# Kernel optimization log

Measured on AMD Instinct MI355X. Metric: run time of the kernel, lower is better.

Reference implementation:

```python
import jax, jax.numpy as jnp
import numpy as np

B, N, D, H = 256, 64, 128, 64

def _w(key, shape, fan_in):
    return jax.random.normal(key, shape, jnp.float32) * (1.0 / np.sqrt(fan_in))

def setup_inputs() -> dict:
    key = jax.random.key(0)
    ks = jax.random.split(key, 6)
    return {
        "observations": jax.random.normal(ks[0], (B, N, D), jnp.float32),
        "enc_w": _w(ks[1], (D, H), D), "enc_b": jnp.zeros((H,), jnp.float32),
        "gate_w1": _w(ks[2], (2 * H, H), 2 * H), "gate_b1": jnp.zeros((H,), jnp.float32),
        "gate_w2": _w(ks[3], (H, 1), H), "gate_b2": jnp.zeros((1,), jnp.float32),
        "msg_w1": _w(ks[4], (H, H), H), "msg_b1": jnp.zeros((H,), jnp.float32),
        "msg_w2": _w(ks[5], (H, H), H), "msg_b2": jnp.zeros((H,), jnp.float32),
    }

def reference(observations, enc_w, enc_b, gate_w1, gate_b1, gate_w2, gate_b2,
              msg_w1, msg_b1, msg_w2, msg_b2):
    # encoder: (B, N, H)
    enc = jax.nn.relu(observations @ enc_w + enc_b)
    h = enc.shape[-1]
    # gate layer 1 on concat([e_i, e_j]) == e_i @ W_top + e_j @ W_bot; avoids
    # materializing the (B, N, N, 2H) concat tensor.
    w_i, w_j = gate_w1[:h], gate_w1[h:]
    gi = enc @ w_i                       # (B, N, H) contribution of receiver i
    gj = enc @ w_j + gate_b1             # (B, N, H) contribution of sender j
    hid = jax.nn.relu(gi[:, :, None, :] + gj[:, None, :, :])   # (B, N, N, H)
    gates = jax.nn.sigmoid(jnp.squeeze(hid @ gate_w2, -1) + gate_b2[0])  # (B, N, N)
    # message_gen(encoded): identical for every i in the original loop
    msg = jax.nn.relu(enc @ msg_w1 + msg_b1) @ msg_w2 + msg_b2  # (B, N, H)
    # enhanced[b, i] = sum_j gates[b, i, j] * msg[b, j]
    enhanced = jnp.einsum('bij,bjh->bih', gates, msg)           # (B, N, H)
    return enhanced
```

## Files before the change

kernel.cpp:

```cpp
#include <hip/hip_runtime.h>

typedef float  f32x4  __attribute__((ext_vector_type(4)));
typedef short  bf16x8 __attribute__((ext_vector_type(8)));

#define Bb 256
#define Nn 64
#define Dd 128
#define Hh 64

__device__ __forceinline__ uint cvtpk(float lo, float hi) {
    uint r;
    asm("v_cvt_pk_bf16_f32 %0, %1, %2" : "=v"(r) : "v"(lo), "v"(hi));
    return r;
}

union U8 { uint u[4]; bf16x8 v; };

__global__ __launch_bounds__(1024) void gcm_kernel(
    const float* __restrict__ obs,
    const float* __restrict__ enc_w,
    const float* __restrict__ enc_b,
    const float* __restrict__ gate_w1,
    const float* __restrict__ gate_b1,
    const float* __restrict__ gate_w2,
    const float* __restrict__ gate_b2,
    const float* __restrict__ msg_w1,
    const float* __restrict__ msg_b1,
    const float* __restrict__ msg_w2,
    const float* __restrict__ msg_b2,
    float* __restrict__ out)
{
    const int bb   = blockIdx.x;
    const int t    = threadIdx.x;
    const int lane = t & 63;
    const int wv   = t >> 6;
    const int lr   = lane & 15;
    const int lg   = lane >> 4;
    const int rt   = wv & 3;
    const int ct   = wv >> 2;

    __shared__ __align__(16) ushort s_encwT[Hh * Dd];
    __shared__ __align__(16) ushort s_wT[256 * Hh];
    __shared__ __align__(16) ushort s_enc  [Nn * Hh];
    __shared__ __align__(16) ushort s_msgh [Nn * Hh];
    __shared__ __align__(16) ushort s_gatesb[Nn * Hh];
    __shared__ __align__(16) ushort s_msgT [Hh * Nn];
    __shared__ __align__(16) float  s_gi[Nn * Hh];
    __shared__ __align__(16) float  s_gj[Nn * Hh];
    __shared__ __align__(16) float  s_w2[Hh];

    float4 pf[8];
    {
        const float* ob = obs + ((size_t)bb * Nn + rt * 16 + lr) * Dd + lg * 8;
        #pragma unroll
        for (int ks = 0; ks < 4; ++ks) {
            pf[2 * ks]     = *(const float4*)(ob + ks * 32);
            pf[2 * ks + 1] = *(const float4*)(ob + ks * 32 + 4);
        }
    }

    if (t < Hh) s_w2[t] = gate_w2[t];

    #pragma unroll
    for (int it = 0; it < 2; ++it) {
        const int g  = t + it * 1024;
        const int k  = g >> 4;
        const int n0 = (g & 15) * 4;
        float4 w4 = *(const float4*)(enc_w + k * Hh + n0);
        uint pA = cvtpk(w4.x, w4.y), pB = cvtpk(w4.z, w4.w);
        s_encwT[((n0 + 0) * Dd + k) ^ (((n0 + 0) & 7) << 3)] = (ushort)pA;
        s_encwT[((n0 + 1) * Dd + k) ^ (((n0 + 1) & 7) << 3)] = (ushort)(pA >> 16);
        s_encwT[((n0 + 2) * Dd + k) ^ (((n0 + 2) & 7) << 3)] = (ushort)pB;
        s_encwT[((n0 + 3) * Dd + k) ^ (((n0 + 3) & 7) << 3)] = (ushort)(pB >> 16);
    }

    bf16x8 afrag[4];
    #pragma unroll
    for (int ks = 0; ks < 4; ++ks) {
        U8 u;
        u.u[0] = cvtpk(pf[2 * ks].x,     pf[2 * ks].y);
        u.u[1] = cvtpk(pf[2 * ks].z,     pf[2 * ks].w);
        u.u[2] = cvtpk(pf[2 * ks + 1].x, pf[2 * ks + 1].y);
        u.u[3] = cvtpk(pf[2 * ks + 1].z, pf[2 * ks + 1].w);
        afrag[ks] = u.v;
    }

    float4 pfw[4];
    {
        const int k  = t >> 4;
        const int n0 = (t & 15) * 4;
        const float* s0 = gate_w1 + k * Hh + n0;
        const float* s1 = gate_w1 + (Hh + k) * Hh + n0;
        const float* s2 = msg_w1 + k * Hh + n0;
        const float* s3 = msg_w2 + k * Hh + n0;
        pfw[0] = *(const float4*)s0;
        pfw[1] = *(const float4*)s1;
        pfw[2] = *(const float4*)s2;
        pfw[3] = *(const float4*)s3;
    }

    __syncthreads();

    {
        f32x4 acc = (f32x4){0.f, 0.f, 0.f, 0.f};
        const int n = ct * 16 + lr;
        #pragma unroll
        for (int ks = 0; ks < 4; ++ks) {
            const int k0 = ks * 32 + lg * 8;
            bf16x8 bf = *(const bf16x8*)(s_encwT + ((n * Dd + k0) ^ ((n & 7) << 3)));
            acc = __builtin_amdgcn_mfma_f32_16x16x32_bf16(afrag[ks], bf, acc, 0, 0, 0);
        }
        #pragma unroll
        for (int it = 0; it < 4; ++it) {
            const int k  = t >> 4;
            const int n0 = it * 64 + (t & 15) * 4;
            uint pA = cvtpk(pfw[it].x, pfw[it].y), pB = cvtpk(pfw[it].z, pfw[it].w);
            s_wT[((n0 + 0) * Hh + k) ^ (((n0 + 0) & 7) << 3)] = (ushort)pA;
            s_wT[((n0 + 1) * Hh + k) ^ (((n0 + 1) & 7) << 3)] = (ushort)(pA >> 16);
            s_wT[((n0 + 2) * Hh + k) ^ (((n0 + 2) & 7) << 3)] = (ushort)pB;
            s_wT[((n0 + 3) * Hh + k) ^ (((n0 + 3) & 7) << 3)] = (ushort)(pB >> 16);
        }
        const float be = enc_b[n];
        float v0 = fmaxf(acc[0] + be, 0.f), v1 = fmaxf(acc[1] + be, 0.f);
        float v2 = fmaxf(acc[2] + be, 0.f), v3 = fmaxf(acc[3] + be, 0.f);
        uint pA = cvtpk(v0, v1), pB = cvtpk(v2, v3);
        const int rb = rt * 16 + lg * 4;
        s_enc[((rb + 0) * Hh + n) ^ (((rb + 0) & 7) << 3)] = (ushort)pA;
        s_enc[((rb + 1) * Hh + n) ^ (((rb + 1) & 7) << 3)] = (ushort)(pA >> 16);
        s_enc[((rb + 2) * Hh + n) ^ (((rb + 2) & 7) << 3)] = (ushort)pB;
        s_enc[((rb + 3) * Hh + n) ^ (((rb + 3) & 7) << 3)] = (ushort)(pB >> 16);
    }
    __syncthreads();

    {
        f32x4 acc[3];
        #pragma unroll
        for (int q = 0; q < 3; ++q) acc[q] = (f32x4){0.f, 0.f, 0.f, 0.f};
        const int arow = rt * 16 + lr;
        #pragma unroll
        for (int ks = 0; ks < 2; ++ks) {
            const int k0 = ks * 32 + lg * 8;
            bf16x8 a = *(const bf16x8*)(s_enc + ((arow * Hh + k0) ^ ((arow & 7) << 3)));
            #pragma unroll
            for (int q = 0; q < 3; ++q) {
                const int n = (ct * 3 + q) * 16 + lr;
                bf16x8 bf = *(const bf16x8*)(s_wT + ((n * Hh + k0) ^ ((n & 7) << 3)));
                acc[q] = __builtin_amdgcn_mfma_f32_16x16x32_bf16(a, bf, acc[q], 0, 0, 0);
            }
        }
        const int rb = rt * 16 + lg * 4;
        #pragma unroll
        for (int q = 0; q < 3; ++q) {
            const int nfull = (ct * 3 + q) * 16;
            const int cc = nfull + lr;
            if (nfull < 64) {
                #pragma unroll
                for (int rr = 0; rr < 4; ++rr) {
                    const int row = rb + rr;
                    s_gi[(row * Hh + cc) ^ ((row & 7) << 2)] = acc[q][rr];
                }
            } else if (nfull < 128) {
                const float b1 = gate_b1[cc - 64];
                #pragma unroll
                for (int rr = 0; rr < 4; ++rr) {
                    const int row = rb + rr;
                    s_gj[(row * Hh + (cc - 64)) ^ ((row & 7) << 2)] = acc[q][rr] + b1;
                }
            } else {
                const float bm = msg_b1[cc - 128];
                float v0 = fmaxf(acc[q][0] + bm, 0.f), v1 = fmaxf(acc[q][1] + bm, 0.f);
                float v2 = fmaxf(acc[q][2] + bm, 0.f), v3 = fmaxf(acc[q][3] + bm, 0.f);
                uint pA = cvtpk(v0, v1), pB = cvtpk(v2, v3);
                const int c2 = cc - 128;
                s_msgh[((rb + 0) * Hh + c2) ^ (((rb + 0) & 7) << 3)] = (ushort)pA;
                s_msgh[((rb + 1) * Hh + c2) ^ (((rb + 1) & 7) << 3)] = (ushort)(pA >> 16);
                s_msgh[((rb + 2) * Hh + c2) ^ (((rb + 2) & 7) << 3)] = (ushort)pB;
                s_msgh[((rb + 3) * Hh + c2) ^ (((rb + 3) & 7) << 3)] = (ushort)(pB >> 16);
            }
        }
    }
    __syncthreads();

    {
        f32x4 acc = (f32x4){0.f, 0.f, 0.f, 0.f};
        const int arow = rt * 16 + lr;
        const int n = 192 + ct * 16 + lr;
        #pragma unroll
        for (int ks = 0; ks < 2; ++ks) {
            const int k0 = ks * 32 + lg * 8;
            bf16x8 a = *(const bf16x8*)(s_msgh + ((arow * Hh + k0) ^ ((arow & 7) << 3)));
            bf16x8 bf = *(const bf16x8*)(s_wT + ((n * Hh + k0) ^ ((n & 7) << 3)));
            acc = __builtin_amdgcn_mfma_f32_16x16x32_bf16(a, bf, acc, 0, 0, 0);
        }
        const int h  = ct * 16 + lr;
        const int jb = rt * 16 + lg * 4;
        const float bm2 = msg_b2[h];
        uint pA = cvtpk(acc[0] + bm2, acc[1] + bm2);
        uint pB = cvtpk(acc[2] + bm2, acc[3] + bm2);
        const int e = (h * Nn + jb) ^ ((h & 7) << 3);
        *(uint*)(s_msgT + e)     = pA;
        *(uint*)(s_msgT + e + 2) = pB;
    }

    {
        const int row0g = wv * 4;
        float ag[4] = {0.f, 0.f, 0.f, 0.f};
        #pragma unroll 4
        for (int h0 = 0; h0 < Hh; h0 += 4) {
            float4 gj4 = *(const float4*)&s_gj[(lane * Hh + h0) ^ ((lane & 7) << 2)];
            float4 w24 = *(const float4*)&s_w2[h0];
            #pragma unroll
            for (int r = 0; r < 4; ++r) {
                const int row = row0g + r;
                float4 gi4 = *(const float4*)&s_gi[(row * Hh + h0) ^ ((row & 7) << 2)];
                ag[r] = fmaf(fmaxf(gi4.x + gj4.x, 0.f), w24.x, ag[r]);
                ag[r] = fmaf(fmaxf(gi4.y + gj4.y, 0.f), w24.y, ag[r]);
                ag[r] = fmaf(fmaxf(gi4.z + gj4.z, 0.f), w24.z, ag[r]);
                ag[r] = fmaf(fmaxf(gi4.w + gj4.w, 0.f), w24.w, ag[r]);
            }
        }
        const float b2v = gate_b2[0];
        float g0 = 1.f / (1.f + __expf(-(ag[0] + b2v)));
        float g1 = 1.f / (1.f + __expf(-(ag[1] + b2v)));
        float g2 = 1.f / (1.f + __expf(-(ag[2] + b2v)));
        float g3 = 1.f / (1.f + __expf(-(ag[3] + b2v)));
        uint pA = cvtpk(g0, g1), pB = cvtpk(g2, g3);
        s_gatesb[((row0g + 0) * Hh + lane) ^ (((row0g + 0) & 7) << 3)] = (ushort)pA;
        s_gatesb[((row0g + 1) * Hh + lane) ^ (((row0g + 1) & 7) << 3)] = (ushort)(pA >> 16);
        s_gatesb[((row0g + 2) * Hh + lane) ^ (((row0g + 2) & 7) << 3)] = (ushort)pB;
        s_gatesb[((row0g + 3) * Hh + lane) ^ (((row0g + 3) & 7) << 3)] = (ushort)(pB >> 16);
    }
    __syncthreads();

    {
        f32x4 acc = (f32x4){0.f, 0.f, 0.f, 0.f};
        const int arow = rt * 16 + lr;
        const int n = ct * 16 + lr;
        #pragma unroll
        for (int ks = 0; ks < 2; ++ks) {
            const int k0 = ks * 32 + lg * 8;
            bf16x8 a = *(const bf16x8*)(s_gatesb + ((arow * Hh + k0) ^ ((arow & 7) << 3)));
            bf16x8 bf = *(const bf16x8*)(s_msgT + ((n * Nn + k0) ^ ((n & 7) << 3)));
            acc = __builtin_amdgcn_mfma_f32_16x16x32_bf16(a, bf, acc, 0, 0, 0);
        }
        const int rb = rt * 16 + lg * 4;
        #pragma unroll
        for (int rr = 0; rr < 4; ++rr)
            out[((size_t)bb * Nn + rb + rr) * Hh + n] = acc[rr];
    }
}

extern "C" void kernel_launch(void* const* d_in, const int* in_sizes, int n_in,
                              void* d_out, int out_size, void* d_ws, size_t ws_size,
                              hipStream_t stream) {
    const float* obs     = (const float*)d_in[0];
    const float* enc_w   = (const float*)d_in[1];
    const float* enc_b   = (const float*)d_in[2];
    const float* gate_w1 = (const float*)d_in[3];
    const float* gate_b1 = (const float*)d_in[4];
    const float* gate_w2 = (const float*)d_in[5];
    const float* gate_b2 = (const float*)d_in[6];
    const float* msg_w1  = (const float*)d_in[7];
    const float* msg_b1  = (const float*)d_in[8];
    const float* msg_w2  = (const float*)d_in[9];
    const float* msg_b2  = (const float*)d_in[10];
    float* out = (float*)d_out;

    gcm_kernel<<<Bb, 1024, 0, stream>>>(obs, enc_w, enc_b, gate_w1, gate_b1,
                                        gate_w2, gate_b2, msg_w1, msg_b1,
                                        msg_w2, msg_b2, out);
}
```

Measured before the change: 21.33 us.

## Split each batch across two 512-thread blocks and alias shared memory

Launches two blocks per batch element, each with 512 threads, and each block computes the gate matrix and output for half of the receiver rows. The encoder and projection stages are still computed in full by both blocks, so that work is duplicated. Shared memory is packed into one aliased arena, and gj is stored as bf16 with padded rows to shrink LDS use and allow more blocks per CU. The aim is better occupancy and shorter per-block critical paths, at the cost of redundant encoder/projection work and bf16 rounding of gj.

```diff
diff --git a/kernel.cpp b/kernel.cpp
--- a/kernel.cpp
+++ b/kernel.cpp
@@ -4,19 +4,19 @@
 typedef short  bf16x8 __attribute__((ext_vector_type(8)));
 
 #define Bb 256
-#define Nn 64
-#define Dd 128
-#define Hh 64
 
 __device__ __forceinline__ uint cvtpk(float lo, float hi) {
     uint r;
     asm("v_cvt_pk_bf16_f32 %0, %1, %2" : "=v"(r) : "v"(lo), "v"(hi));
     return r;
 }
+__device__ __forceinline__ ushort f2b1(float v) { return (ushort)cvtpk(v, v); }
+__device__ __forceinline__ float bflo(uint u) { return __uint_as_float(u << 16); }
+__device__ __forceinline__ float bfhi(uint u) { return __uint_as_float(u & 0xffff0000u); }
 
 union U8 { uint u[4]; bf16x8 v; };
 
-__global__ __launch_bounds__(1024) void gcm_kernel(
+__global__ __launch_bounds__(512, 4) void gcm_kernel(
     const float* __restrict__ obs,
     const float* __restrict__ enc_w,
     const float* __restrict__ enc_b,
@@ -30,50 +30,43 @@
     const float* __restrict__ msg_b2,
     float* __restrict__ out)
 {
-    const int bb   = blockIdx.x;
+    const int bid  = blockIdx.x;
+    const int bb   = bid >> 1;
+    const int half = bid & 1;
     const int t    = threadIdx.x;
     const int lane = t & 63;
     const int wv   = t >> 6;
     const int lr   = lane & 15;
     const int lg   = lane >> 4;
-    const int rt   = wv & 3;
-    const int ct   = wv >> 2;
-
-    __shared__ __align__(16) ushort s_encwT[Hh * Dd];
-    __shared__ __align__(16) ushort s_wT[256 * Hh];
-    __shared__ __align__(16) ushort s_enc  [Nn * Hh];
-    __shared__ __align__(16) ushort s_msgh [Nn * Hh];
-    __shared__ __align__(16) ushort s_gatesb[Nn * Hh];
-    __shared__ __align__(16) ushort s_msgT [Hh * Nn];
-    __shared__ __align__(16) float  s_gi[Nn * Hh];
-    __shared__ __align__(16) float  s_gj[Nn * Hh];
-    __shared__ __align__(16) float  s_w2[Hh];
+    const int rt   = wv >> 1;
+
+    __shared__ __align__(16) char arena[74240];
+    ushort* s_wT     = (ushort*)(arena);
+    ushort* s_encwT  = (ushort*)(arena + 32768);
+    float*  s_gi     = (float*) (arena + 32768);
+    ushort* s_gatesb = (ushort*)(arena + 40960);
+    ushort* s_enc    = (ushort*)(arena + 49152);
+    ushort* s_msgT   = (ushort*)(arena + 49152);
+    ushort* s_msgh   = (ushort*)(arena + 57344);
+    ushort* s_gjb    = (ushort*)(arena + 65536);
 
     float4 pf[8];
     {
-        const float* ob = obs + ((size_t)bb * Nn + rt * 16 + lr) * Dd + lg * 8;
+        const float* ob = obs + ((size_t)bb * 64 + rt * 16 + lr) * 128 + lg * 8;
         #pragma unroll
         for (int ks = 0; ks < 4; ++ks) {
             pf[2 * ks]     = *(const float4*)(ob + ks * 32);
             pf[2 * ks + 1] = *(const float4*)(ob + ks * 32 + 4);
         }
     }
-
-    if (t < Hh) s_w2[t] = gate_w2[t];
-
+    float4 pe[4];
     #pragma unroll
-    for (int it = 0; it < 2; ++it) {
-        const int g  = t + it * 1024;
-        const int k  = g >> 4;
-        const int n0 = (g & 15) * 4;
-        float4 w4 = *(const float4*)(enc_w + k * Hh + n0);
-        uint pA = cvtpk(w4.x, w4.y), pB = cvtpk(w4.z, w4.w);
-        s_encwT[((n0 + 0) * Dd + k) ^ (((n0 + 0) & 7) << 3)] = (ushort)pA;
-        s_encwT[((n0 + 1) * Dd + k) ^ (((n0 + 1) & 7) << 3)] = (ushort)(pA >> 16);
-        s_encwT[((n0 + 2) * Dd + k) ^ (((n0 + 2) & 7) << 3)] = (ushort)pB;
-        s_encwT[((n0 + 3) * Dd + k) ^ (((n0 + 3) & 7) << 3)] = (ushort)(pB >> 16);
-    }
-
+    for (int it = 0; it < 4; ++it) {
+        const int idx = t + it * 512;
+        const int k   = idx >> 4;
+        const int n0  = (idx & 15) * 4;
+        pe[it] = *(const float4*)(enc_w + k * 64 + n0);
+    }
     bf16x8 afrag[4];
     #pragma unroll
     for (int ks = 0; ks < 4; ++ks) {
@@ -84,169 +77,212 @@
         u.u[3] = cvtpk(pf[2 * ks + 1].z, pf[2 * ks + 1].w);
         afrag[ks] = u.v;
     }
-
-    float4 pfw[4];
+    #pragma unroll
+    for (int it = 0; it < 4; ++it) {
+        const int idx = t + it * 512;
+        const int k   = idx >> 4;
+        const int n0  = (idx & 15) * 4;
+        uint pA = cvtpk(pe[it].x, pe[it].y), pB = cvtpk(pe[it].z, pe[it].w);
+        s_encwT[((n0 + 0) * 128 + k) ^ (((n0 + 0) & 7) << 3)] = (ushort)pA;
+        s_encwT[((n0 + 1) * 128 + k) ^ (((n0 + 1) & 7) << 3)] = (ushort)(pA >> 16);
+        s_encwT[((n0 + 2) * 128 + k) ^ (((n0 + 2) & 7) << 3)] = (ushort)pB;
+        s_encwT[((n0 + 3) * 128 + k) ^ (((n0 + 3) & 7) << 3)] = (ushort)(pB >> 16);
+    }
+    float4 pfw[8];
     {
         const int k  = t >> 4;
         const int n0 = (t & 15) * 4;
-        const float* s0 = gate_w1 + k * Hh + n0;
-        const float* s1 = gate_w1 + (Hh + k) * Hh + n0;
-        const float* s2 = msg_w1 + k * Hh + n0;
-        const float* s3 = msg_w2 + k * Hh + n0;
-        pfw[0] = *(const float4*)s0;
-        pfw[1] = *(const float4*)s1;
-        pfw[2] = *(const float4*)s2;
-        pfw[3] = *(const float4*)s3;
-    }
-
+        #pragma unroll
+        for (int kh = 0; kh < 2; ++kh) {
+            const int kk = k + kh * 32;
+            pfw[0 * 2 + kh] = *(const float4*)(gate_w1 + kk * 64 + n0);
+            pfw[1 * 2 + kh] = *(const float4*)(gate_w1 + (64 + kk) * 64 + n0);
+            pfw[2 * 2 + kh] = *(const float4*)(msg_w1 + kk * 64 + n0);
+            pfw[3 * 2 + kh] = *(const float4*)(msg_w2 + kk * 64 + n0);
+        }
+    }
     __syncthreads();
 
     {
-        f32x4 acc = (f32x4){0.f, 0.f, 0.f, 0.f};
-        const int n = ct * 16 + lr;
+        f32x4 acc[2];
+        acc[0] = (f32x4){0.f, 0.f, 0.f, 0.f};
+        acc[1] = (f32x4){0.f, 0.f, 0.f, 0.f};
         #pragma unroll
         for (int ks = 0; ks < 4; ++ks) {
             const int k0 = ks * 32 + lg * 8;
-            bf16x8 bf = *(const bf16x8*)(s_encwT + ((n * Dd + k0) ^ ((n & 7) << 3)));
-            acc = __builtin_amdgcn_mfma_f32_16x16x32_bf16(afrag[ks], bf, acc, 0, 0, 0);
-        }
-        #pragma unroll
-        for (int it = 0; it < 4; ++it) {
+            #pragma unroll
+            for (int jj = 0; jj < 2; ++jj) {
+                const int n = (wv & 1) * 32 + jj * 16 + lr;
+                bf16x8 bf = *(const bf16x8*)(s_encwT + ((n * 128 + k0) ^ ((n & 7) << 3)));
+                acc[jj] = __builtin_amdgcn_mfma_f32_16x16x32_bf16(afrag[ks], bf, acc[jj], 0, 0, 0);
+            }
+        }
+        {
             const int k  = t >> 4;
-            const int n0 = it * 64 + (t & 15) * 4;
-            uint pA = cvtpk(pfw[it].x, pfw[it].y), pB = cvtpk(pfw[it].z, pfw[it].w);
-            s_wT[((n0 + 0) * Hh + k) ^ (((n0 + 0) & 7) << 3)] = (ushort)pA;
-            s_wT[((n0 + 1) * Hh + k) ^ (((n0 + 1) & 7) << 3)] = (ushort)(pA >> 16);
-            s_wT[((n0 + 2) * Hh + k) ^ (((n0 + 2) & 7) << 3)] = (ushort)pB;
-            s_wT[((n0 + 3) * Hh + k) ^ (((n0 + 3) & 7) << 3)] = (ushort)(pB >> 16);
-        }
-        const float be = enc_b[n];
-        float v0 = fmaxf(acc[0] + be, 0.f), v1 = fmaxf(acc[1] + be, 0.f);
-        float v2 = fmaxf(acc[2] + be, 0.f), v3 = fmaxf(acc[3] + be, 0.f);
-        uint pA = cvtpk(v0, v1), pB = cvtpk(v2, v3);
+            const int n00 = (t & 15) * 4;
+            #pragma unroll
+            for (int m = 0; m < 4; ++m) {
+                #pragma unroll
+                for (int kh = 0; kh < 2; ++kh) {
+                    float4 w4 = pfw[m * 2 + kh];
+                    const int kk = k + kh * 32;
+                    const int nb = m * 64 + n00;
+                    uint pA = cvtpk(w4.x, w4.y), pB = cvtpk(w4.z, w4.w);
+                    s_wT[((nb + 0) * 64 + kk) ^ (((nb + 0) & 7) << 3)] = (ushort)pA;
+                    s_wT[((nb + 1) * 64 + kk) ^ (((nb + 1) & 7) << 3)] = (ushort)(pA >> 16);
+                    s_wT[((nb + 2) * 64 + kk) ^ (((nb + 2) & 7) << 3)] = (ushort)pB;
+                    s_wT[((nb + 3) * 64 + kk) ^ (((nb + 3) & 7) << 3)] = (ushort)(pB >> 16);
+                }
+            }
+        }
         const int rb = rt * 16 + lg * 4;
-        s_enc[((rb + 0) * Hh + n) ^ (((rb + 0) & 7) << 3)] = (ushort)pA;
-        s_enc[((rb + 1) * Hh + n) ^ (((rb + 1) & 7) << 3)] = (ushort)(pA >> 16);
-        s_enc[((rb + 2) * Hh + n) ^ (((rb + 2) & 7) << 3)] = (ushort)pB;
-        s_enc[((rb + 3) * Hh + n) ^ (((rb + 3) & 7) << 3)] = (ushort)(pB >> 16);
+        #pragma unroll
+        for (int jj = 0; jj < 2; ++jj) {
+            const int n = (wv & 1) * 32 + jj * 16 + lr;
+            const float be = enc_b[n];
+            #pragma unroll
+            for (int rr = 0; rr < 4; ++rr) {
+                const int row = rb + rr;
+                float v = fmaxf(acc[jj][rr] + be, 0.f);
+                s_enc[(row * 64 + n) ^ ((row & 7) << 3)] = f2b1(v);
+            }
+        }
     }
     __syncthreads();
 
     {
-        f32x4 acc[3];
-        #pragma unroll
-        for (int q = 0; q < 3; ++q) acc[q] = (f32x4){0.f, 0.f, 0.f, 0.f};
+        f32x4 acc[6];
+        #pragma unroll
+        for (int q = 0; q < 6; ++q) acc[q] = (f32x4){0.f, 0.f, 0.f, 0.f};
         const int arow = rt * 16 + lr;
         #pragma unroll
         for (int ks = 0; ks < 2; ++ks) {
             const int k0 = ks * 32 + lg * 8;
-            bf16x8 a = *(const bf16x8*)(s_enc + ((arow * Hh + k0) ^ ((arow & 7) << 3)));
-            #pragma unroll
-            for (int q = 0; q < 3; ++q) {
-                const int n = (ct * 3 + q) * 16 + lr;
-                bf16x8 bf = *(const bf16x8*)(s_wT + ((n * Hh + k0) ^ ((n & 7) << 3)));
+            bf16x8 a = *(const bf16x8*)(s_enc + ((arow * 64 + k0) ^ ((arow & 7) << 3)));
+            #pragma unroll
+            for (int q = 0; q < 6; ++q) {
+                const int n = ((wv & 1) * 6 + q) * 16 + lr;
+                bf16x8 bf = *(const bf16x8*)(s_wT + ((n * 64 + k0) ^ ((n & 7) << 3)));
                 acc[q] = __builtin_amdgcn_mfma_f32_16x16x32_bf16(a, bf, acc[q], 0, 0, 0);
             }
         }
         const int rb = rt * 16 + lg * 4;
         #pragma unroll
-        for (int q = 0; q < 3; ++q) {
-            const int nfull = (ct * 3 + q) * 16;
+        for (int q = 0; q < 6; ++q) {
+            const int nfull = ((wv & 1) * 6 + q) * 16;
             const int cc = nfull + lr;
             if (nfull < 64) {
-                #pragma unroll
-                for (int rr = 0; rr < 4; ++rr) {
-                    const int row = rb + rr;
-                    s_gi[(row * Hh + cc) ^ ((row & 7) << 2)] = acc[q][rr];
+                if ((rt >> 1) == half) {
+                    const int lb = rb - half * 32;
+                    #pragma unroll
+                    for (int rr = 0; rr < 4; ++rr) {
+                        const int row = lb + rr;
+                        s_gi[(row * 64 + cc) ^ ((row & 7) << 2)] = acc[q][rr];
+                    }
                 }
             } else if (nfull < 128) {
                 const float b1 = gate_b1[cc - 64];
                 #pragma unroll
-                for (int rr = 0; rr < 4; ++rr) {
-                    const int row = rb + rr;
-                    s_gj[(row * Hh + (cc - 64)) ^ ((row & 7) << 2)] = acc[q][rr] + b1;
-                }
+                for (int rr = 0; rr < 4; ++rr)
+                    s_gjb[(rb + rr) * 68 + (cc - 64)] = f2b1(acc[q][rr] + b1);
             } else {
                 const float bm = msg_b1[cc - 128];
                 float v0 = fmaxf(acc[q][0] + bm, 0.f), v1 = fmaxf(acc[q][1] + bm, 0.f);
                 float v2 = fmaxf(acc[q][2] + bm, 0.f), v3 = fmaxf(acc[q][3] + bm, 0.f);
                 uint pA = cvtpk(v0, v1), pB = cvtpk(v2, v3);
                 const int c2 = cc - 128;
-                s_msgh[((rb + 0) * Hh + c2) ^ (((rb + 0) & 7) << 3)] = (ushort)pA;
-                s_msgh[((rb + 1) * Hh + c2) ^ (((rb + 1) & 7) << 3)] = (ushort)(pA >> 16);
-                s_msgh[((rb + 2) * Hh + c2) ^ (((rb + 2) & 7) << 3)] = (ushort)pB;
-                s_msgh[((rb + 3) * Hh + c2) ^ (((rb + 3) & 7) << 3)] = (ushort)(pB >> 16);
+                s_msgh[((rb + 0) * 64 + c2) ^ (((rb + 0) & 7) << 3)] = (ushort)pA;
+                s_msgh[((rb + 1) * 64 + c2) ^ (((rb + 1) & 7) << 3)] = (ushort)(pA >> 16);
+                s_msgh[((rb + 2) * 64 + c2) ^ (((rb + 2) & 7) << 3)] = (ushort)pB;
+                s_msgh[((rb + 3) * 64 + c2) ^ (((rb + 3) & 7) << 3)] = (ushort)(pB >> 16);
             }
         }
     }
     __syncthreads();
 
     {
-        f32x4 acc = (f32x4){0.f, 0.f, 0.f, 0.f};
+        f32x4 acc[2];
+        acc[0] = (f32x4){0.f, 0.f, 0.f, 0.f};
+        acc[1] = (f32x4){0.f, 0.f, 0.f, 0.f};
         const int arow = rt * 16 + lr;
-        const int n = 192 + ct * 16 + lr;
         #pragma unroll
         for (int ks = 0; ks < 2; ++ks) {
             const int k0 = ks * 32 + lg * 8;
-            bf16x8 a = *(const bf16x8*)(s_msgh + ((arow * Hh + k0) ^ ((arow & 7) << 3)));
-            bf16x8 bf = *(const bf16x8*)(s_wT + ((n * Hh + k0) ^ ((n & 7) << 3)));
-            acc = __builtin_amdgcn_mfma_f32_16x16x32_bf16(a, bf, acc, 0, 0, 0);
-        }
-        const int h  = ct * 16 + lr;
+            bf16x8 a = *(const bf16x8*)(s_msgh + ((arow * 64 + k0) ^ ((arow & 7) << 3)));
+            #pragma unroll
+            for (int jj = 0; jj < 2; ++jj) {
+                const int n = 192 + ((wv & 1) * 2 + jj) * 16 + lr;
+                bf16x8 bf = *(const bf16x8*)(s_wT + ((n * 64 + k0) ^ ((n & 7) << 3)));
+                acc[jj] = __builtin_amdgcn_mfma_f32_16x16x32_bf16(a, bf, acc[jj], 0, 0, 0);
+            }
+        }
         const int jb = rt * 16 + lg * 4;
-        const float bm2 = msg_b2[h];
-        uint pA = cvtpk(acc[0] + bm2, acc[1] + bm2);
-        uint pB = cvtpk(acc[2] + bm2, acc[3] + bm2);
-        const int e = (h * Nn + jb) ^ ((h & 7) << 3);
-        *(uint*)(s_msgT + e)     = pA;
-        *(uint*)(s_msgT + e + 2) = pB;
-    }
-
-    {
-        const int row0g = wv * 4;
+        #pragma unroll
+        for (int jj = 0; jj < 2; ++jj) {
+            const int h = ((wv & 1) * 2 + jj) * 16 + lr;
+            const float bm2 = msg_b2[h];
+            uint pA = cvtpk(acc[jj][0] + bm2, acc[jj][1] + bm2);
+            uint pB = cvtpk(acc[jj][2] + bm2, acc[jj][3] + bm2);
+            const int e = (h * 64 + jb) ^ ((h & 7) << 3);
+            *(uint*)(s_msgT + e)     = pA;
+            *(uint*)(s_msgT + e + 2) = pB;
+        }
+    }
+
+    {
+        const int lrow0 = wv * 4;
         float ag[4] = {0.f, 0.f, 0.f, 0.f};
-        #pragma unroll 4
-        for (int h0 = 0; h0 < Hh; h0 += 4) {
-            float4 gj4 = *(const float4*)&s_gj[(lane * Hh + h0) ^ ((lane & 7) << 2)];
-            float4 w24 = *(const float4*)&s_w2[h0];
+        const ushort* gjrow = s_gjb + lane * 68;
+        #pragma unroll
+        for (int h0 = 0; h0 < 64; h0 += 8) {
+            uint2 pj0 = *(const uint2*)(gjrow + h0);
+            uint2 pj1 = *(const uint2*)(gjrow + h0 + 4);
+            float gj0 = bflo(pj0.x), gj1 = bfhi(pj0.x), gj2 = bflo(pj0.y), gj3 = bfhi(pj0.y);
+            float gj4 = bflo(pj1.x), gj5 = bfhi(pj1.x), gj6 = bflo(pj1.y), gj7 = bfhi(pj1.y);
+            float4 w2a = *(const float4*)(gate_w2 + h0);
+            float4 w2b = *(const float4*)(gate_w2 + h0 + 4);
             #pragma unroll
             for (int r = 0; r < 4; ++r) {
-                const int row = row0g + r;
-                float4 gi4 = *(const float4*)&s_gi[(row * Hh + h0) ^ ((row & 7) << 2)];
-                ag[r] = fmaf(fmaxf(gi4.x + gj4.x, 0.f), w24.x, ag[r]);
-                ag[r] = fmaf(fmaxf(gi4.y + gj4.y, 0.f), w24.y, ag[r]);
-                ag[r] = fmaf(fmaxf(gi4.z + gj4.z, 0.f), w24.z, ag[r]);
-                ag[r] = fmaf(fmaxf(gi4.w + gj4.w, 0.f), w24.w, ag[r]);
+                const int row = lrow0 + r;
+                float4 gia = *(const float4*)(s_gi + ((row * 64 + h0) ^ ((row & 7) << 2)));
+                float4 gib = *(const float4*)(s_gi + ((row * 64 + h0 + 4) ^ ((row & 7) << 2)));
+                ag[r] = fmaf(fmaxf(gia.x + gj0, 0.f), w2a.x, ag[r]);
+                ag[r] = fmaf(fmaxf(gia.y + gj1, 0.f), w2a.y, ag[r]);
+                ag[r] = fmaf(fmaxf(gia.z + gj2, 0.f), w2a.z, ag[r]);
+                ag[r] = fmaf(fmaxf(gia.w + gj3, 0.f), w2a.w, ag[r]);
+                ag[r] = fmaf(fmaxf(gib.x + gj4, 0.f), w2b.x, ag[r]);
+                ag[r] = fmaf(fmaxf(gib.y + gj5, 0.f), w2b.y, ag[r]);
+                ag[r] = fmaf(fmaxf(gib.z + gj6, 0.f), w2b.z, ag[r]);
+                ag[r] = fmaf(fmaxf(gib.w + gj7, 0.f), w2b.w, ag[r]);
             }
         }
         const float b2v = gate_b2[0];
-        float g0 = 1.f / (1.f + __expf(-(ag[0] + b2v)));
-        float g1 = 1.f / (1.f + __expf(-(ag[1] + b2v)));
-        float g2 = 1.f / (1.f + __expf(-(ag[2] + b2v)));
-        float g3 = 1.f / (1.f + __expf(-(ag[3] + b2v)));
-        uint pA = cvtpk(g0, g1), pB = cvtpk(g2, g3);
-        s_gatesb[((row0g + 0) * Hh + lane) ^ (((row0g + 0) & 7) << 3)] = (ushort)pA;
-        s_gatesb[((row0g + 1) * Hh + lane) ^ (((row0g + 1) & 7) << 3)] = (ushort)(pA >> 16);
-        s_gatesb[((row0g + 2) * Hh + lane) ^ (((row0g + 2) & 7) << 3)] = (ushort)pB;
-        s_gatesb[((row0g + 3) * Hh + lane) ^ (((row0g + 3) & 7) << 3)] = (ushort)(pB >> 16);
+        #pragma unroll
+        for (int r = 0; r < 4; ++r) {
+            const int row = lrow0 + r;
+            const float g = 1.f / (1.f + __expf(-(ag[r] + b2v)));
+            s_gatesb[(row * 64 + lane) ^ ((row & 7) << 3)] = f2b1(g);
+        }
     }
     __syncthreads();
 
     {
+        const int rtl = wv >> 2;
+        const int ct  = wv & 3;
         f32x4 acc = (f32x4){0.f, 0.f, 0.f, 0.f};
-        const int arow = rt * 16 + lr;
+        const int arow = rtl * 16 + lr;
         const int n = ct * 16 + lr;
         #pragma unroll
         for (int ks = 0; ks < 2; ++ks) {
             const int k0 = ks * 32 + lg * 8;
-            bf16x8 a = *(const bf16x8*)(s_gatesb + ((arow * Hh + k0) ^ ((arow & 7) << 3)));
-            bf16x8 bf = *(const bf16x8*)(s_msgT + ((n * Nn + k0) ^ ((n & 7) << 3)));
+            bf16x8 a  = *(const bf16x8*)(s_gatesb + ((arow * 64 + k0) ^ ((arow & 7) << 3)));
+            bf16x8 bf = *(const bf16x8*)(s_msgT   + ((n * 64 + k0) ^ ((n & 7) << 3)));
             acc = __builtin_amdgcn_mfma_f32_16x16x32_bf16(a, bf, acc, 0, 0, 0);
         }
-        const int rb = rt * 16 + lg * 4;
+        const int rb = half * 32 + rtl * 16 + lg * 4;
         #pragma unroll
         for (int rr = 0; rr < 4; ++rr)
-            out[((size_t)bb * Nn + rb + rr) * Hh + n] = acc[rr];
+            out[((size_t)bb * 64 + rb + rr) * 64 + n] = acc[rr];
     }
 }
 
@@ -266,7 +302,7 @@
     const float* msg_b2  = (const float*)d_in[10];
     float* out = (float*)d_out;
 
-    gcm_kernel<<<Bb, 1024, 0, stream>>>(obs, enc_w, enc_b, gate_w1, gate_b1,
-                                        gate_w2, gate_b2, msg_w1, msg_b1,
-                                        msg_w2, msg_b2, out);
+    gcm_kernel<<<2 * Bb, 512, 0, stream>>>(obs, enc_w, enc_b, gate_w1, gate_b1,
+                                           gate_w2, gate_b2, msg_w1, msg_b1,
+                                           msg_w2, msg_b2, out);
 }
```

After: 22.33 us. +4.7%, slower.
